# Performance work log

Hardware: AMD Instinct MI355X
Metric: run time of the kernel (lower is better)

## Reference

```python
import jax, jax.numpy as jnp
import numpy as np

N = 4_000_000
N_COEF = 18  # Tolles-Lawson coefficient count
LAMBDA_PHY = 1.0


def setup_inputs() -> dict:
    key = jax.random.key(0)
    k1, k2, k3, k4, k5 = jax.random.split(key, 5)
    return {
        "model_output": jax.random.normal(k1, (N, N_COEF + 1), dtype=jnp.float32),
        "y": jax.random.normal(k2, (N, 1), dtype=jnp.float32),
        "A": jax.random.normal(k3, (N, N_COEF), dtype=jnp.float32),
        "B_tl": jax.random.normal(k4, (N, 1), dtype=jnp.float32),
        "beta_TL": jax.random.normal(k5, (N_COEF,), dtype=jnp.float32),
    }


def reference(model_output, y, A, B_tl, beta_TL):
    # c: [N,18] per-sample coefficient corrections; d: [N,1] additive bias
    c = model_output[:, :N_COEF]
    d = model_output[:, N_COEF:N_COEF + 1]
    # diag(A @ (beta+c).T) == row-wise dot product sum(A * (beta+c), axis=1)
    tmp_value = jnp.sum(A * (beta_TL + c), axis=1, keepdims=True) + d  # [N,1]
    L_data = jnp.mean(jnp.square(tmp_value - y))
    L_TLprior = jnp.mean(jnp.square(tmp_value - B_tl))
    return L_data + LAMBDA_PHY * L_TLprior
```

## Files before the change

### kernel.cpp

```cpp
#include <hip/hip_runtime.h>

#define NCOEF 18
#define TILE 256
#define GRID1 2048

__global__ __launch_bounds__(256) void loss_partial_kernel(
    const float* __restrict__ mo,
    const float* __restrict__ y,
    const float* __restrict__ A,
    const float* __restrict__ Btl,
    const float* __restrict__ beta,
    float2* __restrict__ partial,
    int N, int numTiles)
{
    __shared__ __align__(16) float s_mo[TILE * 19];
    __shared__ __align__(16) float s_a [TILE * 18];
    __shared__ __align__(16) float s_y [TILE];
    __shared__ __align__(16) float s_b [TILE];
    __shared__ float2 s_red[TILE / 64];

    const int tid = threadIdx.x;

    float bcoef[NCOEF];
#pragma unroll
    for (int j = 0; j < NCOEF; ++j) bcoef[j] = beta[j];

    float s1 = 0.0f, s2 = 0.0f;

    for (int t = blockIdx.x; t < numTiles; t += gridDim.x) {
        const int base = t * TILE;
        const int rows = min(TILE, N - base);

        {
            const int nf = rows * 19;
            const float4* src = reinterpret_cast<const float4*>(mo + (size_t)base * 19);
            float4* dst = reinterpret_cast<float4*>(s_mo);
            for (int i = tid; i < (nf >> 2); i += TILE) dst[i] = src[i];
            for (int i = (nf & ~3) + tid; i < nf; i += TILE)
                s_mo[i] = mo[(size_t)base * 19 + i];
        }
        {
            const int nf = rows * 18;
            const float4* src = reinterpret_cast<const float4*>(A + (size_t)base * 18);
            float4* dst = reinterpret_cast<float4*>(s_a);
            for (int i = tid; i < (nf >> 2); i += TILE) dst[i] = src[i];
            for (int i = (nf & ~3) + tid; i < nf; i += TILE)
                s_a[i] = A[(size_t)base * 18 + i];
        }
        {
            const float4* srcy = reinterpret_cast<const float4*>(y + base);
            const float4* srcb = reinterpret_cast<const float4*>(Btl + base);
            float4* dsty = reinterpret_cast<float4*>(s_y);
            float4* dstb = reinterpret_cast<float4*>(s_b);
            for (int i = tid; i < (rows >> 2); i += TILE) { dsty[i] = srcy[i]; dstb[i] = srcb[i]; }
            for (int i = (rows & ~3) + tid; i < rows; i += TILE) {
                s_y[i] = y[base + i];
                s_b[i] = Btl[base + i];
            }
        }
        __syncthreads();

        if (tid < rows) {
            float tmp = s_mo[tid * 19 + NCOEF];
#pragma unroll
            for (int j = 0; j < NCOEF; ++j)
                tmp = fmaf(s_a[tid * 18 + j], bcoef[j] + s_mo[tid * 19 + j], tmp);
            const float e1 = tmp - s_y[tid];
            const float e2 = tmp - s_b[tid];
            s1 = fmaf(e1, e1, s1);
            s2 = fmaf(e2, e2, s2);
        }
        __syncthreads();
    }

#pragma unroll
    for (int off = 32; off > 0; off >>= 1) {
        s1 += __shfl_down(s1, off);
        s2 += __shfl_down(s2, off);
    }
    if ((tid & 63) == 0) s_red[tid >> 6] = make_float2(s1, s2);
    __syncthreads();
    if (tid == 0) {
        float a1 = 0.0f, a2 = 0.0f;
#pragma unroll
        for (int w = 0; w < TILE / 64; ++w) { a1 += s_red[w].x; a2 += s_red[w].y; }
        partial[blockIdx.x] = make_float2(a1, a2);
    }
}

__global__ __launch_bounds__(256) void loss_final_kernel(
    const float2* __restrict__ partial, int nPart,
    float* __restrict__ out, float invN)
{
    __shared__ float2 s_red[4];
    float s1 = 0.0f, s2 = 0.0f;
    for (int i = threadIdx.x; i < nPart; i += 256) {
        const float2 p = partial[i];
        s1 += p.x; s2 += p.y;
    }
#pragma unroll
    for (int off = 32; off > 0; off >>= 1) {
        s1 += __shfl_down(s1, off);
        s2 += __shfl_down(s2, off);
    }
    if ((threadIdx.x & 63) == 0) s_red[threadIdx.x >> 6] = make_float2(s1, s2);
    __syncthreads();
    if (threadIdx.x == 0) {
        float a1 = 0.0f, a2 = 0.0f;
#pragma unroll
        for (int w = 0; w < 4; ++w) { a1 += s_red[w].x; a2 += s_red[w].y; }
        out[0] = (a1 + a2) * invN;
    }
}

extern "C" void kernel_launch(void* const* d_in, const int* in_sizes, int n_in,
                              void* d_out, int out_size, void* d_ws, size_t ws_size,
                              hipStream_t stream) {
    const float* mo   = (const float*)d_in[0];
    const float* y    = (const float*)d_in[1];
    const float* A    = (const float*)d_in[2];
    const float* Btl  = (const float*)d_in[3];
    const float* beta = (const float*)d_in[4];
    float* out = (float*)d_out;

    const int N = in_sizes[1];
    const int numTiles = (N + TILE - 1) / TILE;
    const int g1 = numTiles < GRID1 ? numTiles : GRID1;

    float2* partial = (float2*)d_ws;

    loss_partial_kernel<<<g1, TILE, 0, stream>>>(mo, y, A, Btl, beta, partial, N, numTiles);
    loss_final_kernel<<<1, 256, 0, stream>>>(partial, g1, out, 1.0f / (float)N);
}
```

Baseline: 579.4 us.

## Stage tiles via direct global-to-LDS loads and read y/B_tl from global

Replaces the register-staged float4 copy loops with global_load_lds 16-byte direct-to-LDS loads for model_output and A. Each wave loads interleaved 1 KB chunks. y and B_tl are now read directly from global memory, and the partial last tile is handled separately so the main loop needs no bounds checks. This is meant to cut VGPR traffic and per-tile instruction overhead, and the launch bounds now request 4 blocks per CU. Each tile still waits with vmcnt(0) and a barrier, so there is no double-buffering overlap.

```diff
diff --git a/kernel.cpp b/kernel.cpp
--- a/kernel.cpp
+++ b/kernel.cpp
@@ -2,75 +2,83 @@
 
 #define NCOEF 18
 #define TILE 256
+#define NWAVES 4
 #define GRID1 2048
 
-__global__ __launch_bounds__(256) void loss_partial_kernel(
+typedef unsigned int u32;
+
+__device__ __forceinline__ void gload_lds16(const void* g, void* l) {
+    __builtin_amdgcn_global_load_lds(
+        (const __attribute__((address_space(1))) u32*)g,
+        (__attribute__((address_space(3))) u32*)l,
+        16, 0, 0);
+}
+
+__global__ __launch_bounds__(256, 4) void loss_partial_kernel(
     const float* __restrict__ mo,
     const float* __restrict__ y,
     const float* __restrict__ A,
     const float* __restrict__ Btl,
     const float* __restrict__ beta,
     float2* __restrict__ partial,
-    int N, int numTiles)
+    int numFullTiles, int N)
 {
     __shared__ __align__(16) float s_mo[TILE * 19];
     __shared__ __align__(16) float s_a [TILE * 18];
-    __shared__ __align__(16) float s_y [TILE];
-    __shared__ __align__(16) float s_b [TILE];
-    __shared__ float2 s_red[TILE / 64];
+    __shared__ float2 s_red[NWAVES];
 
-    const int tid = threadIdx.x;
+    const int tid  = threadIdx.x;
+    const int lane = tid & 63;
+    const int wave = tid >> 6;
 
-    float bcoef[NCOEF];
+    float bc[NCOEF];
 #pragma unroll
-    for (int j = 0; j < NCOEF; ++j) bcoef[j] = beta[j];
+    for (int j = 0; j < NCOEF; ++j) bc[j] = beta[j];
 
     float s1 = 0.0f, s2 = 0.0f;
 
-    for (int t = blockIdx.x; t < numTiles; t += gridDim.x) {
-        const int base = t * TILE;
-        const int rows = min(TILE, N - base);
+    for (int t = blockIdx.x; t < numFullTiles; t += gridDim.x) {
+        const size_t R0 = (size_t)t * TILE;
 
-        {
-            const int nf = rows * 19;
-            const float4* src = reinterpret_cast<const float4*>(mo + (size_t)base * 19);
-            float4* dst = reinterpret_cast<float4*>(s_mo);
-            for (int i = tid; i < (nf >> 2); i += TILE) dst[i] = src[i];
-            for (int i = (nf & ~3) + tid; i < nf; i += TILE)
-                s_mo[i] = mo[(size_t)base * 19 + i];
-        }
-        {
-            const int nf = rows * 18;
-            const float4* src = reinterpret_cast<const float4*>(A + (size_t)base * 18);
-            float4* dst = reinterpret_cast<float4*>(s_a);
-            for (int i = tid; i < (nf >> 2); i += TILE) dst[i] = src[i];
-            for (int i = (nf & ~3) + tid; i < nf; i += TILE)
-                s_a[i] = A[(size_t)base * 18 + i];
-        }
-        {
-            const float4* srcy = reinterpret_cast<const float4*>(y + base);
-            const float4* srcb = reinterpret_cast<const float4*>(Btl + base);
-            float4* dsty = reinterpret_cast<float4*>(s_y);
-            float4* dstb = reinterpret_cast<float4*>(s_b);
-            for (int i = tid; i < (rows >> 2); i += TILE) { dsty[i] = srcy[i]; dstb[i] = srcb[i]; }
-            for (int i = (rows & ~3) + tid; i < rows; i += TILE) {
-                s_y[i] = y[base + i];
-                s_b[i] = Btl[base + i];
-            }
-        }
+        const char* mo_src = (const char*)(mo + R0 * 19) + lane * 16;
+        const char* a_src  = (const char*)(A  + R0 * 18) + lane * 16;
+
+#pragma unroll
+        for (int c = wave; c < 19; c += NWAVES)
+            gload_lds16(mo_src + c * 1024, (char*)s_mo + c * 1024);
+#pragma unroll
+        for (int c = wave; c < 18; c += NWAVES)
+            gload_lds16(a_src + c * 1024, (char*)s_a + c * 1024);
+
+        asm volatile("s_waitcnt vmcnt(0)" ::: "memory");
         __syncthreads();
 
-        if (tid < rows) {
-            float tmp = s_mo[tid * 19 + NCOEF];
+        float tmp = s_mo[tid * 19 + NCOEF];
 #pragma unroll
-            for (int j = 0; j < NCOEF; ++j)
-                tmp = fmaf(s_a[tid * 18 + j], bcoef[j] + s_mo[tid * 19 + j], tmp);
-            const float e1 = tmp - s_y[tid];
-            const float e2 = tmp - s_b[tid];
-            s1 = fmaf(e1, e1, s1);
-            s2 = fmaf(e2, e2, s2);
-        }
+        for (int j = 0; j < NCOEF; ++j)
+            tmp = fmaf(s_a[tid * 18 + j], bc[j] + s_mo[tid * 19 + j], tmp);
+
+        const float yv = y[R0 + tid];
+        const float bv = Btl[R0 + tid];
+        const float e1 = tmp - yv;
+        const float e2 = tmp - bv;
+        s1 = fmaf(e1, e1, s1);
+        s2 = fmaf(e2, e2, s2);
+
         __syncthreads();
+    }
+
+    const int rem = N - numFullTiles * TILE;
+    if (rem > 0 && blockIdx.x == gridDim.x - 1 && tid < rem) {
+        const size_t r = (size_t)numFullTiles * TILE + tid;
+        float tmp = mo[r * 19 + NCOEF];
+#pragma unroll
+        for (int j = 0; j < NCOEF; ++j)
+            tmp = fmaf(A[r * 18 + j], bc[j] + mo[r * 19 + j], tmp);
+        const float e1 = tmp - y[r];
+        const float e2 = tmp - Btl[r];
+        s1 = fmaf(e1, e1, s1);
+        s2 = fmaf(e2, e2, s2);
     }
 
 #pragma unroll
@@ -78,12 +86,12 @@
         s1 += __shfl_down(s1, off);
         s2 += __shfl_down(s2, off);
     }
-    if ((tid & 63) == 0) s_red[tid >> 6] = make_float2(s1, s2);
+    if (lane == 0) s_red[wave] = make_float2(s1, s2);
     __syncthreads();
     if (tid == 0) {
         float a1 = 0.0f, a2 = 0.0f;
 #pragma unroll
-        for (int w = 0; w < TILE / 64; ++w) { a1 += s_red[w].x; a2 += s_red[w].y; }
+        for (int w = 0; w < NWAVES; ++w) { a1 += s_red[w].x; a2 += s_red[w].y; }
         partial[blockIdx.x] = make_float2(a1, a2);
     }
 }
@@ -124,11 +132,13 @@
     float* out = (float*)d_out;
 
     const int N = in_sizes[1];
-    const int numTiles = (N + TILE - 1) / TILE;
-    const int g1 = numTiles < GRID1 ? numTiles : GRID1;
+    const int numFullTiles = N / TILE;
+    int g1 = numFullTiles < GRID1 ? numFullTiles : GRID1;
+    if (g1 < 1) g1 = 1;
 
     float2* partial = (float2*)d_ws;
 
-    loss_partial_kernel<<<g1, TILE, 0, stream>>>(mo, y, A, Btl, beta, partial, N, numTiles);
+    loss_partial_kernel<<<g1, TILE, 0, stream>>>(mo, y, A, Btl, beta, partial,
+                                                 numFullTiles, N);
     loss_final_kernel<<<1, 256, 0, stream>>>(partial, g1, out, 1.0f / (float)N);
 }
```

Measured after the change: 578.4 us. No clear change (-0.2%).
